# Optimization experiments

Hardware: AMD Instinct MI355X
Metric: run time of the kernel (lower is better)

Reference implementation:

```python
import jax, jax.numpy as jnp
import numpy as np

N, B, T, D = 4, 4, 512, 512
H, DK, DV = 8, 64, 64
LN_EPS = 1e-5


def setup_inputs() -> dict:
    key = jax.random.key(0)
    ks = jax.random.split(key, 5)
    s = 1.0 / np.sqrt(D)
    return {
        "x": jax.random.normal(ks[0], (N, B, T, D), jnp.float32),
        "Wq": jax.random.normal(ks[1], (D, H * DK), jnp.float32) * s,
        "bq": jnp.zeros((H * DK,), jnp.float32),
        "Wk": jax.random.normal(ks[2], (D, H * DK), jnp.float32) * s,
        "bk": jnp.zeros((H * DK,), jnp.float32),
        "Wv": jax.random.normal(ks[3], (D, H * DV), jnp.float32) * s,
        "bv": jnp.zeros((H * DV,), jnp.float32),
        "Wo": jax.random.normal(ks[4], (H * DV, D), jnp.float32) * (1.0 / np.sqrt(H * DV)),
        "bo": jnp.zeros((D,), jnp.float32),
        "gamma": jnp.ones((D,), jnp.float32),
        "beta": jnp.zeros((D,), jnp.float32),
    }


def reference(x, Wq, bq, Wk, bk, Wv, bv, Wo, bo, gamma, beta):
    # x: [N, B, T, D] -- N variables, each [B, T, D]
    n = x.shape[0]
    # Project once per variable (the torch code redundantly recomputes K/V per query var).
    q = (x @ Wq + bq).reshape(n, B, T, H, DK).transpose(0, 1, 3, 2, 4)  # [N,B,H,T,DK]
    k = (x @ Wk + bk).reshape(n, B, T, H, DK).transpose(0, 1, 3, 2, 4)  # [N,B,H,T,DK]
    v = (x @ Wv + bv).reshape(n, B, T, H, DV).transpose(0, 1, 3, 2, 4)  # [N,B,H,T,DV]
    # All-pairs attention: softmax over keys of EACH key-variable separately.
    scores = jnp.einsum('qbhtk,cbhsk->qcbhts', q, k) / np.sqrt(DK)  # [Nq,Nc,B,H,T,T]
    attn = jax.nn.softmax(scores, axis=-1)
    ctx = jnp.einsum('qcbhts,cbhsv->qcbhtv', attn, v)  # [Nq,Nc,B,H,T,DV]
    ctx = ctx.transpose(0, 1, 2, 4, 3, 5).reshape(n, n, B, T, H * DV)
    out = ctx @ Wo + bo                     # per-pair output projection
    out = out.sum(axis=1) / n               # average over key variables -> [N,B,T,D]
    res = x + out
    mu = res.mean(axis=-1, keepdims=True)
    var = res.var(axis=-1, keepdims=True)
    y = (res - mu) / jnp.sqrt(var + LN_EPS) * gamma + beta
    return y
```

## Files before the change

### kernel.cpp

```cpp
#include <hip/hip_runtime.h>


typedef __bf16 bf16x8 __attribute__((ext_vector_type(8)));
typedef __bf16 bf16x4 __attribute__((ext_vector_type(4)));
typedef short shortx4 __attribute__((ext_vector_type(4)));
typedef float floatx2 __attribute__((ext_vector_type(2)));
typedef float floatx4 __attribute__((ext_vector_type(4)));
typedef float floatx16 __attribute__((ext_vector_type(16)));
typedef unsigned short ushortx8 __attribute__((ext_vector_type(8)));
typedef unsigned int uintx4 __attribute__((ext_vector_type(4)));

static __device__ __forceinline__ unsigned short f2bf(float f) {
  union { __bf16 h; unsigned short u; } c; c.h = (__bf16)f; return c.u;
}
static __device__ __forceinline__ float bf2f(unsigned short u) {
  union { unsigned u32; float f; } c; c.u32 = ((unsigned)u) << 16; return c.f;
}
static __device__ __forceinline__ unsigned cvtpk(float a, float b) {
  unsigned r;
  asm("v_cvt_pk_bf16_f32 %0, %1, %2" : "=v"(r) : "v"(a), "v"(b));
  return r;
}
static __device__ __forceinline__ void barrier_lgkm() {
  asm volatile("s_waitcnt lgkmcnt(0)\n\ts_barrier" ::: "memory");
}

#define QSCALE 0.18033688011112042f
#define SHIFT2 (-17.312340489609306f)

__global__ __launch_bounds__(256) void prep(
    const float* __restrict__ Wq, const float* __restrict__ Wk,
    const float* __restrict__ Wv, const float* __restrict__ Wo,
    const float* __restrict__ x,
    unsigned short* __restrict__ wqkvT, unsigned short* __restrict__ woT,
    unsigned short* __restrict__ x_bf)
{
  const int bid = blockIdx.x;
  const int tid = threadIdx.x;
  if (bid < 256) {
    __shared__ unsigned short lds[64][65];
    const int z = bid >> 6, rest = bid & 63;
    const int k0 = (rest >> 3) * 64, n0 = (rest & 7) * 64;
    const float* W; unsigned short* T;
    if (z == 0)      { W = Wq; T = wqkvT; }
    else if (z == 1) { W = Wk; T = wqkvT + 262144; }
    else if (z == 2) { W = Wv; T = wqkvT + 524288; }
    else             { W = Wo; T = woT; }
    const int xx = tid & 63, yy = tid >> 6;
#pragma unroll
    for (int i = 0; i < 16; ++i) {
      const int row = yy * 16 + i;
      lds[row][xx] = f2bf(W[(size_t)(k0 + row) * 512 + n0 + xx]);
    }
    __syncthreads();
#pragma unroll
    for (int i = 0; i < 16; ++i) {
      const int nr = yy * 16 + i;
      T[(size_t)(n0 + nr) * 512 + k0 + xx] = lds[xx][nr];
    }
  } else {
    const int i = (bid - 256) * 256 + tid;
    const float4 a = ((const float4*)x)[i * 2];
    const float4 b = ((const float4*)x)[i * 2 + 1];
    ushortx8 o;
    o[0] = f2bf(a.x); o[1] = f2bf(a.y); o[2] = f2bf(a.z); o[3] = f2bf(a.w);
    o[4] = f2bf(b.x); o[5] = f2bf(b.y); o[6] = f2bf(b.z); o[7] = f2bf(b.w);
    *(ushortx8*)(x_bf + (size_t)i * 8) = o;
  }
}

__global__ __launch_bounds__(256) void gemm_qkv(
    const unsigned short* __restrict__ Xb,
    const unsigned short* __restrict__ BT,
    const float* __restrict__ bq, const float* __restrict__ bk,
    const float* __restrict__ bv,
    unsigned short* __restrict__ Qo, unsigned short* __restrict__ Ko,
    unsigned short* __restrict__ Vo)
{
  __shared__ __align__(16) unsigned short sbuf[18432];
  auto lA = (unsigned short (*)[72])sbuf;
  auto lB = (unsigned short (*)[72])(sbuf + 9216);
  const int tid  = threadIdx.x;
  const int wv   = tid >> 6, lane = tid & 63;
  const int quad = lane >> 4, l16 = lane & 15;
  const int wm = wv >> 1, wn = wv & 1;
  const int m0  = blockIdx.x * 128;
  const int n0g = blockIdx.y * 128;
  const int sel = n0g >> 9;
  const float* bias = (sel == 0) ? bq : (sel == 1) ? bk : bv;
  const float scale = (sel == 0) ? QSCALE : 1.0f;
  unsigned short* outp = (sel == 0) ? Qo : (sel == 1) ? Ko : Vo;

  floatx4 acc[4][4] = {};
  const int srow = tid >> 1, sc0 = (tid & 1) * 32;

  for (int kc = 0; kc < 512; kc += 64) {
    __syncthreads();
    const unsigned short* as = Xb + (size_t)(m0 + srow) * 512 + kc + sc0;
    const unsigned short* bs = BT + (size_t)(n0g + srow) * 512 + kc + sc0;
#pragma unroll
    for (int j = 0; j < 4; ++j) {
      *(bf16x8*)&lA[srow][sc0 + j * 8] = *(const bf16x8*)(as + j * 8);
      *(bf16x8*)&lB[srow][sc0 + j * 8] = *(const bf16x8*)(bs + j * 8);
    }
    __syncthreads();
    bf16x8 af[4][2];
#pragma unroll
    for (int ti = 0; ti < 4; ++ti) {
      af[ti][0] = *(const bf16x8*)&lA[wm * 64 + ti * 16 + l16][quad * 8];
      af[ti][1] = *(const bf16x8*)&lA[wm * 64 + ti * 16 + l16][32 + quad * 8];
    }
#pragma unroll
    for (int ni = 0; ni < 4; ++ni) {
      bf16x8 b0 = *(const bf16x8*)&lB[wn * 64 + ni * 16 + l16][quad * 8];
      bf16x8 b1 = *(const bf16x8*)&lB[wn * 64 + ni * 16 + l16][32 + quad * 8];
#pragma unroll
      for (int ti = 0; ti < 4; ++ti) {
        acc[ti][ni] = __builtin_amdgcn_mfma_f32_16x16x32_bf16(af[ti][0], b0, acc[ti][ni], 0, 0, 0);
        acc[ti][ni] = __builtin_amdgcn_mfma_f32_16x16x32_bf16(af[ti][1], b1, acc[ti][ni], 0, 0, 0);
      }
    }
  }

  if (sel != 2) {
#pragma unroll
    for (int ni = 0; ni < 4; ++ni) {
      const int n = (n0g & 511) + wn * 64 + ni * 16 + l16;
      const float bvv = bias[n];
      const int hh = n >> 6, dk = n & 63;
#pragma unroll
      for (int ti = 0; ti < 4; ++ti) {
        const int mb = m0 + wm * 64 + ti * 16 + quad * 4;
#pragma unroll
        for (int r = 0; r < 4; ++r) {
          const int m = mb + r;
          const int nb = m >> 9, t = m & 511;
          outp[((size_t)(nb * 8 + hh) * 512 + t) * 64 + dk] =
              f2bf((acc[ti][ni][r] + bvv) * scale);
        }
      }
    }
  } else {
    __syncthreads();
    auto tb = (unsigned short (*)[136])sbuf;
#pragma unroll
    for (int ni = 0; ni < 4; ++ni) {
      const int n = (n0g & 511) + wn * 64 + ni * 16 + l16;
      const float bvv = bias[n];
      const int drow = wn * 64 + ni * 16 + l16;
#pragma unroll
      for (int ti = 0; ti < 4; ++ti) {
        const int tcol = wm * 64 + ti * 16 + quad * 4;
        shortx4 pk;
        pk[0] = (short)f2bf(acc[ti][ni][0] + bvv);
        pk[1] = (short)f2bf(acc[ti][ni][1] + bvv);
        pk[2] = (short)f2bf(acc[ti][ni][2] + bvv);
        pk[3] = (short)f2bf(acc[ti][ni][3] + bvv);
        *(shortx4*)&tb[drow][tcol] = pk;
      }
    }
    __syncthreads();
    const int drow = tid >> 1, th = tid & 1;
    const int n = (n0g & 511) + drow;
    const int hh = n >> 6, dk = n & 63;
    const int nb = m0 >> 9, tbase = (m0 & 511) + th * 64;
    unsigned short* gdst = outp + ((size_t)(nb * 8 + hh) * 64 + dk) * 512 + tbase;
#pragma unroll
    for (int j = 0; j < 8; ++j)
      *(ushortx8*)(gdst + j * 8) = *(const ushortx8*)&tb[drow][th * 64 + j * 8];
  }
}

__global__ __launch_bounds__(256) void gemm_out(
    const unsigned short* __restrict__ C0, const unsigned short* __restrict__ C1,
    const unsigned short* __restrict__ BT, unsigned short* __restrict__ Cout)
{
  __shared__ __align__(16) unsigned short lA[128][72];
  __shared__ __align__(16) unsigned short lB[128][72];
  const int tid  = threadIdx.x;
  const int wv   = tid >> 6, lane = tid & 63;
  const int quad = lane >> 4, l16 = lane & 15;
  const int wm = wv >> 1, wn = wv & 1;
  const int m0 = blockIdx.x * 128, n0 = blockIdx.y * 128;

  floatx4 acc[4][4] = {};
  const int srow = tid >> 1, sc0 = (tid & 1) * 32;

  for (int kc = 0; kc < 512; kc += 64) {
    __syncthreads();
    const size_t aoff = (size_t)(m0 + srow) * 512 + kc + sc0;
    const unsigned short* bs = BT + (size_t)(n0 + srow) * 512 + kc + sc0;
#pragma unroll
    for (int j = 0; j < 4; ++j) {
      ushortx8 a0 = *(const ushortx8*)(C0 + aoff + j * 8);
      ushortx8 a1 = *(const ushortx8*)(C1 + aoff + j * 8);
      ushortx8 o;
#pragma unroll
      for (int e = 0; e < 8; ++e) o[e] = f2bf(bf2f(a0[e]) + bf2f(a1[e]));
      *(ushortx8*)&lA[srow][sc0 + j * 8] = o;
      *(bf16x8*)&lB[srow][sc0 + j * 8] = *(const bf16x8*)(bs + j * 8);
    }
    __syncthreads();
    bf16x8 af[4][2];
#pragma unroll
    for (int ti = 0; ti < 4; ++ti) {
      af[ti][0] = *(const bf16x8*)&lA[wm * 64 + ti * 16 + l16][quad * 8];
      af[ti][1] = *(const bf16x8*)&lA[wm * 64 + ti * 16 + l16][32 + quad * 8];
    }
#pragma unroll
    for (int ni = 0; ni < 4; ++ni) {
      bf16x8 b0 = *(const bf16x8*)&lB[wn * 64 + ni * 16 + l16][quad * 8];
      bf16x8 b1 = *(const bf16x8*)&lB[wn * 64 + ni * 16 + l16][32 + quad * 8];
#pragma unroll
      for (int ti = 0; ti < 4; ++ti) {
        acc[ti][ni] = __builtin_amdgcn_mfma_f32_16x16x32_bf16(af[ti][0], b0, acc[ti][ni], 0, 0, 0);
        acc[ti][ni] = __builtin_amdgcn_mfma_f32_16x16x32_bf16(af[ti][1], b1, acc[ti][ni], 0, 0, 0);
      }
    }
  }

#pragma unroll
  for (int ni = 0; ni < 4; ++ni) {
    const int n = n0 + wn * 64 + ni * 16 + l16;
#pragma unroll
    for (int ti = 0; ti < 4; ++ti) {
      const int mb = m0 + wm * 64 + ti * 16 + quad * 4;
#pragma unroll
      for (int r = 0; r < 4; ++r)
        Cout[(size_t)(mb + r) * 512 + n] = f2bf(acc[ti][ni][r]);
    }
  }
}

__global__ __launch_bounds__(256) void flash_kernel(
    const unsigned short* __restrict__ Q,
    const unsigned short* __restrict__ K,
    const unsigned short* __restrict__ VT,
    unsigned short* __restrict__ CTX2)
{
  __shared__ __align__(16) unsigned short lK[2][64][72];
  __shared__ __align__(16) unsigned short lV[2][64][68];
  const int tid  = threadIdx.x;
  const int wv   = tid >> 6, lane = tid & 63;
  const int l32  = lane & 31, u = lane >> 5;

  const int lin  = blockIdx.x;
  const int xcd  = lin & 7, slot = lin >> 3;
  const int tile = slot & 3;
  const int nbh  = xcd * 16 + ((slot >> 2) & 15);
  const int cg   = slot >> 6;
  const int t0   = tile * 128;
  const int h = nbh & 7, nb = nbh >> 3, b = nb & 3;

  const unsigned short* qbase = Q + ((size_t)nbh * 512 + (t0 + wv * 32 + l32)) * 64;
  bf16x8 qf[4];
#pragma unroll
  for (int c16 = 0; c16 < 4; ++c16)
    qf[c16] = *(const bf16x8*)(qbase + c16 * 16 + u * 8);

  const int srow = tid >> 2, sc0 = (tid & 3) * 16;
  const unsigned short *kptr, *vptr;
  auto setptr = [&](int it) {
    const int c = cg * 2 + (it >> 3), s0 = (it & 7) * 64;
    const size_t kvbh = (size_t)((c * 4 + b) * 8 + h);
    kptr = K  + kvbh * (512 * 64) + (size_t)(s0 + srow) * 64 + sc0;
    vptr = VT + kvbh * (64 * 512) + (size_t)srow * 512 + s0 + sc0;
  };
  bf16x8 rk0, rk1, rv0, rv1;
  auto loadregs = [&]() {
    rk0 = *(const bf16x8*)kptr; rk1 = *(const bf16x8*)(kptr + 8);
    rv0 = *(const bf16x8*)vptr; rv1 = *(const bf16x8*)(vptr + 8);
  };
  auto writebuf = [&](int p) {
    *(bf16x8*)&lK[p][srow][sc0]     = rk0;
    *(bf16x8*)&lK[p][srow][sc0 + 8] = rk1;
    union { bf16x8 v8; bf16x4 v4[2]; } c0, c1;
    c0.v8 = rv0; c1.v8 = rv1;
    *(bf16x4*)&lV[p][srow][sc0]      = c0.v4[0];
    *(bf16x4*)&lV[p][srow][sc0 + 4]  = c0.v4[1];
    *(bf16x4*)&lV[p][srow][sc0 + 8]  = c1.v4[0];
    *(bf16x4*)&lV[p][srow][sc0 + 12] = c1.v4[1];
  };

  setptr(0); loadregs();
  writebuf(0);
  setptr(1); loadregs();
  barrier_lgkm();

  floatx16 ofin0 = {}, ofin1 = {};
  floatx16 oc0, oc1;
  floatx2 lac2;

  for (int it = 0; it < 16; ++it) {
    const int cur = it & 1;
    const int st = it & 7;
    if (st == 0) { oc0 = floatx16{}; oc1 = floatx16{}; lac2 = floatx2{}; }

    if (it < 15) writebuf(cur ^ 1);
    if (it < 14) { setptr(it + 2); loadregs(); }

    __builtin_amdgcn_s_setprio(1);
#pragma unroll
    for (int sb = 0; sb < 2; ++sb) {
      floatx16 sacc;
#pragma unroll
      for (int r = 0; r < 16; ++r) sacc[r] = SHIFT2;
#pragma unroll
      for (int c16 = 0; c16 < 4; ++c16) {
        bf16x8 ak = *(const bf16x8*)&lK[cur][sb * 32 + l32][c16 * 16 + u * 8];
        sacc = __builtin_amdgcn_mfma_f32_32x32x16_bf16(ak, qf[c16], sacc, 0, 0, 0);
      }
#pragma unroll
      for (int g = 0; g < 2; ++g) {
        float e[8];
#pragma unroll
        for (int j = 0; j < 8; ++j) e[j] = __builtin_amdgcn_exp2f(sacc[8 * g + j]);
        floatx2 s01 = floatx2{e[0], e[1]} + floatx2{e[2], e[3]};
        floatx2 s23 = floatx2{e[4], e[5]} + floatx2{e[6], e[7]};
        lac2 += s01 + s23;
        union { unsigned u32[4]; bf16x8 b8; } pf;
        pf.u32[0] = cvtpk(e[0], e[1]);
        pf.u32[1] = cvtpk(e[2], e[3]);
        pf.u32[2] = cvtpk(e[4], e[5]);
        pf.u32[3] = cvtpk(e[6], e[7]);
        const int slA = sb * 32 + g * 16 + u * 4;
        union { shortx4 s4[2]; bf16x8 b8; } va, vb;
        va.s4[0] = *(const shortx4*)&lV[cur][l32][slA];
        va.s4[1] = *(const shortx4*)&lV[cur][l32][slA + 8];
        vb.s4[0] = *(const shortx4*)&lV[cur][32 + l32][slA];
        vb.s4[1] = *(const shortx4*)&lV[cur][32 + l32][slA + 8];
        oc0 = __builtin_amdgcn_mfma_f32_32x32x16_bf16(pf.b8, va.b8, oc0, 0, 0, 0);
        oc1 = __builtin_amdgcn_mfma_f32_32x32x16_bf16(pf.b8, vb.b8, oc1, 0, 0, 0);
      }
    }
    __builtin_amdgcn_s_setprio(0);

    if (st == 7) {
      float s = lac2[0] + lac2[1];
      s += __shfl_xor(s, 32);
      const float inv = 1.0f / s;
#pragma unroll
      for (int r = 0; r < 16; ++r) {
        const int trow = (r & 3) + 8 * (r >> 2) + 4 * u;
        const float invr = __shfl(inv, trow);
        ofin0[r] += oc0[r] * invr;
        ofin1[r] += oc1[r] * invr;
      }
    }
    barrier_lgkm();
  }

  unsigned short* outp = CTX2 + (size_t)cg * (8192 * 512);
  const int mbase = nb * 512 + t0 + wv * 32;
#pragma unroll
  for (int r = 0; r < 16; ++r) {
    const int trow = (r & 3) + 8 * (r >> 2) + 4 * u;
    const size_t rowoff = (size_t)(mbase + trow) * 512 + h * 64;
    outp[rowoff + l32]      = f2bf(ofin0[r]);
    outp[rowoff + 32 + l32] = f2bf(ofin1[r]);
  }
}

__global__ __launch_bounds__(256) void ln_kernel(
    const float* __restrict__ x, const unsigned short* __restrict__ tmpb,
    const float* __restrict__ bo, const float* __restrict__ gamma,
    const float* __restrict__ beta, float* __restrict__ out)
{
  const int wv   = threadIdx.x >> 6, lane = threadIdx.x & 63;
  const int row  = blockIdx.x * 4 + wv;
  const int col  = lane * 8;
  const size_t base = (size_t)row * 512 + col;
  const float4 x0 = *(const float4*)(x + base);
  const float4 x1 = *(const float4*)(x + base + 4);
  const ushortx8 t8 = *(const ushortx8*)(tmpb + base);
  const float4 b0 = *(const float4*)(bo + col);
  const float4 b1 = *(const float4*)(bo + col + 4);
  float r[8];
  r[0] = x0.x + 0.25f * bf2f(t8[0]) + b0.x;  r[1] = x0.y + 0.25f * bf2f(t8[1]) + b0.y;
  r[2] = x0.z + 0.25f * bf2f(t8[2]) + b0.z;  r[3] = x0.w + 0.25f * bf2f(t8[3]) + b0.w;
  r[4] = x1.x + 0.25f * bf2f(t8[4]) + b1.x;  r[5] = x1.y + 0.25f * bf2f(t8[5]) + b1.y;
  r[6] = x1.z + 0.25f * bf2f(t8[6]) + b1.z;  r[7] = x1.w + 0.25f * bf2f(t8[7]) + b1.w;
  float s = 0.f, sq = 0.f;
#pragma unroll
  for (int j = 0; j < 8; ++j) { s += r[j]; sq += r[j] * r[j]; }
#pragma unroll
  for (int off = 1; off < 64; off <<= 1) {
    s  += __shfl_xor(s, off);
    sq += __shfl_xor(sq, off);
  }
  const float mu  = s * (1.0f / 512.0f);
  const float var = sq * (1.0f / 512.0f) - mu * mu;
  const float inv = rsqrtf(var + 1e-5f);
  const float4 g0 = *(const float4*)(gamma + col);
  const float4 g1 = *(const float4*)(gamma + col + 4);
  const float4 be0 = *(const float4*)(beta + col);
  const float4 be1 = *(const float4*)(beta + col + 4);
  float4 o0, o1;
  o0.x = (r[0] - mu) * inv * g0.x + be0.x;  o0.y = (r[1] - mu) * inv * g0.y + be0.y;
  o0.z = (r[2] - mu) * inv * g0.z + be0.z;  o0.w = (r[3] - mu) * inv * g0.w + be0.w;
  o1.x = (r[4] - mu) * inv * g1.x + be1.x;  o1.y = (r[5] - mu) * inv * g1.y + be1.y;
  o1.z = (r[6] - mu) * inv * g1.z + be1.z;  o1.w = (r[7] - mu) * inv * g1.w + be1.w;
  *(float4*)(out + base)     = o0;
  *(float4*)(out + base + 4) = o1;
}

extern "C" void kernel_launch(void* const* d_in, const int* in_sizes, int n_in,
                              void* d_out, int out_size, void* d_ws, size_t ws_size,
                              hipStream_t stream) {
  const float* x     = (const float*)d_in[0];
  const float* Wq    = (const float*)d_in[1];
  const float* bq    = (const float*)d_in[2];
  const float* Wk    = (const float*)d_in[3];
  const float* bk    = (const float*)d_in[4];
  const float* Wv    = (const float*)d_in[5];
  const float* bv    = (const float*)d_in[6];
  const float* Wo    = (const float*)d_in[7];
  const float* bo    = (const float*)d_in[8];
  const float* gamma = (const float*)d_in[9];
  const float* beta  = (const float*)d_in[10];
  float* out = (float*)d_out;

  char* w = (char*)d_ws;
  unsigned short* q_bf  = (unsigned short*)(w);
  unsigned short* k_bf  = (unsigned short*)(w + (size_t)8  * 1024 * 1024);
  unsigned short* vt_bf = (unsigned short*)(w + (size_t)16 * 1024 * 1024);
  unsigned short* x_bf  = (unsigned short*)(w + (size_t)24 * 1024 * 1024);
  unsigned short* ctx2  = (unsigned short*)(w + (size_t)24 * 1024 * 1024);
  unsigned short* wqkvT = (unsigned short*)(w + (size_t)40 * 1024 * 1024);
  unsigned short* woT   = wqkvT + 786432;
  unsigned short* tmpb  = (unsigned short*)(w);

  prep<<<2304, 256, 0, stream>>>(Wq, Wk, Wv, Wo, x, wqkvT, woT, x_bf);
  gemm_qkv<<<dim3(64, 12), 256, 0, stream>>>(x_bf, wqkvT, bq, bk, bv,
                                             q_bf, k_bf, vt_bf);
  flash_kernel<<<1024, 256, 0, stream>>>(q_bf, k_bf, vt_bf, ctx2);
  gemm_out<<<dim3(64, 4), 256, 0, stream>>>(ctx2, ctx2 + (size_t)8192 * 512,
                                            woT, tmpb);
  ln_kernel<<<2048, 256, 0, stream>>>(x, tmpb, bo, gamma, beta, out);
}
```

Measured before the change: 189.3 us.

## Split flash attention per key-variable into 2048 blocks with four-way ctx reduction

When the workspace allows, the flash kernel assigns each block one key variable instead of two, doubling the grid to 2048 blocks. Each block writes its own normalized context slice to one of four buffers. The output GEMM then sums the four bf16 context slices while staging the A tile. This gives more parallelism and a shorter serial loop per block, at the cost of a larger intermediate buffer, more global memory traffic, and an extra bf16 rounding before the sum.

```diff
diff --git a/kernel.cpp b/kernel.cpp
--- a/kernel.cpp
+++ b/kernel.cpp
@@ -171,7 +171,72 @@
   }
 }
 
-__global__ __launch_bounds__(256) void gemm_out(
+__global__ __launch_bounds__(256) void gemm_out4(
+    const unsigned short* __restrict__ C0, const unsigned short* __restrict__ C1,
+    const unsigned short* __restrict__ C2, const unsigned short* __restrict__ C3,
+    const unsigned short* __restrict__ BT, unsigned short* __restrict__ Cout)
+{
+  __shared__ __align__(16) unsigned short lA[128][72];
+  __shared__ __align__(16) unsigned short lB[128][72];
+  const int tid  = threadIdx.x;
+  const int wv   = tid >> 6, lane = tid & 63;
+  const int quad = lane >> 4, l16 = lane & 15;
+  const int wm = wv >> 1, wn = wv & 1;
+  const int m0 = blockIdx.x * 128, n0 = blockIdx.y * 128;
+
+  floatx4 acc[4][4] = {};
+  const int srow = tid >> 1, sc0 = (tid & 1) * 32;
+
+  for (int kc = 0; kc < 512; kc += 64) {
+    __syncthreads();
+    const size_t aoff = (size_t)(m0 + srow) * 512 + kc + sc0;
+    const unsigned short* bs = BT + (size_t)(n0 + srow) * 512 + kc + sc0;
+#pragma unroll
+    for (int j = 0; j < 4; ++j) {
+      ushortx8 a0 = *(const ushortx8*)(C0 + aoff + j * 8);
+      ushortx8 a1 = *(const ushortx8*)(C1 + aoff + j * 8);
+      ushortx8 a2 = *(const ushortx8*)(C2 + aoff + j * 8);
+      ushortx8 a3 = *(const ushortx8*)(C3 + aoff + j * 8);
+      ushortx8 o;
+#pragma unroll
+      for (int e = 0; e < 8; ++e)
+        o[e] = f2bf((bf2f(a0[e]) + bf2f(a1[e])) + (bf2f(a2[e]) + bf2f(a3[e])));
+      *(ushortx8*)&lA[srow][sc0 + j * 8] = o;
+      *(bf16x8*)&lB[srow][sc0 + j * 8] = *(const bf16x8*)(bs + j * 8);
+    }
+    __syncthreads();
+    bf16x8 af[4][2];
+#pragma unroll
+    for (int ti = 0; ti < 4; ++ti) {
+      af[ti][0] = *(const bf16x8*)&lA[wm * 64 + ti * 16 + l16][quad * 8];
+      af[ti][1] = *(const bf16x8*)&lA[wm * 64 + ti * 16 + l16][32 + quad * 8];
+    }
+#pragma unroll
+    for (int ni = 0; ni < 4; ++ni) {
+      bf16x8 b0 = *(const bf16x8*)&lB[wn * 64 + ni * 16 + l16][quad * 8];
+      bf16x8 b1 = *(const bf16x8*)&lB[wn * 64 + ni * 16 + l16][32 + quad * 8];
+#pragma unroll
+      for (int ti = 0; ti < 4; ++ti) {
+        acc[ti][ni] = __builtin_amdgcn_mfma_f32_16x16x32_bf16(af[ti][0], b0, acc[ti][ni], 0, 0, 0);
+        acc[ti][ni] = __builtin_amdgcn_mfma_f32_16x16x32_bf16(af[ti][1], b1, acc[ti][ni], 0, 0, 0);
+      }
+    }
+  }
+
+#pragma unroll
+  for (int ni = 0; ni < 4; ++ni) {
+    const int n = n0 + wn * 64 + ni * 16 + l16;
+#pragma unroll
+    for (int ti = 0; ti < 4; ++ti) {
+      const int mb = m0 + wm * 64 + ti * 16 + quad * 4;
+#pragma unroll
+      for (int r = 0; r < 4; ++r)
+        Cout[(size_t)(mb + r) * 512 + n] = f2bf(acc[ti][ni][r]);
+    }
+  }
+}
+
+__global__ __launch_bounds__(256) void gemm_out2(
     const unsigned short* __restrict__ C0, const unsigned short* __restrict__ C1,
     const unsigned short* __restrict__ BT, unsigned short* __restrict__ Cout)
 {
@@ -232,7 +297,128 @@
   }
 }
 
-__global__ __launch_bounds__(256) void flash_kernel(
+__global__ __launch_bounds__(256) void flash_c1(
+    const unsigned short* __restrict__ Q,
+    const unsigned short* __restrict__ K,
+    const unsigned short* __restrict__ VT,
+    unsigned short* __restrict__ CTX4)
+{
+  __shared__ __align__(16) unsigned short lK[2][64][72];
+  __shared__ __align__(16) unsigned short lV[2][64][68];
+  const int tid  = threadIdx.x;
+  const int wv   = tid >> 6, lane = tid & 63;
+  const int l32  = lane & 31, u = lane >> 5;
+
+  const int lin  = blockIdx.x;
+  const int xcd  = lin & 7, slot = lin >> 3;
+  const int tile = slot & 3;
+  const int nbh  = xcd * 16 + ((slot >> 2) & 15);
+  const int c    = slot >> 6;
+  const int t0   = tile * 128;
+  const int h = nbh & 7, nb = nbh >> 3, b = nb & 3;
+
+  const unsigned short* qbase = Q + ((size_t)nbh * 512 + (t0 + wv * 32 + l32)) * 64;
+  bf16x8 qf[4];
+#pragma unroll
+  for (int c16 = 0; c16 < 4; ++c16)
+    qf[c16] = *(const bf16x8*)(qbase + c16 * 16 + u * 8);
+
+  const int srow = tid >> 2, sc0 = (tid & 3) * 16;
+  const size_t kvbh = (size_t)((c * 4 + b) * 8 + h);
+  const unsigned short* kb = K  + kvbh * (512 * 64);
+  const unsigned short* vb = VT + kvbh * (64 * 512);
+  const unsigned short *kptr, *vptr;
+  auto setptr = [&](int it) {
+    const int s0 = it * 64;
+    kptr = kb + (size_t)(s0 + srow) * 64 + sc0;
+    vptr = vb + (size_t)srow * 512 + s0 + sc0;
+  };
+  bf16x8 rk0, rk1, rv0, rv1;
+  auto loadregs = [&]() {
+    rk0 = *(const bf16x8*)kptr; rk1 = *(const bf16x8*)(kptr + 8);
+    rv0 = *(const bf16x8*)vptr; rv1 = *(const bf16x8*)(vptr + 8);
+  };
+  auto writebuf = [&](int p) {
+    *(bf16x8*)&lK[p][srow][sc0]     = rk0;
+    *(bf16x8*)&lK[p][srow][sc0 + 8] = rk1;
+    union { bf16x8 v8; bf16x4 v4[2]; } c0, c1;
+    c0.v8 = rv0; c1.v8 = rv1;
+    *(bf16x4*)&lV[p][srow][sc0]      = c0.v4[0];
+    *(bf16x4*)&lV[p][srow][sc0 + 4]  = c0.v4[1];
+    *(bf16x4*)&lV[p][srow][sc0 + 8]  = c1.v4[0];
+    *(bf16x4*)&lV[p][srow][sc0 + 12] = c1.v4[1];
+  };
+
+  setptr(0); loadregs();
+  writebuf(0);
+  setptr(1); loadregs();
+  barrier_lgkm();
+
+  floatx16 oc0 = {}, oc1 = {};
+  floatx2 lac2 = {};
+
+  for (int it = 0; it < 8; ++it) {
+    const int cur = it & 1;
+
+    if (it < 7) writebuf(cur ^ 1);
+    if (it < 6) { setptr(it + 2); loadregs(); }
+
+    __builtin_amdgcn_s_setprio(1);
+#pragma unroll
+    for (int sb = 0; sb < 2; ++sb) {
+      floatx16 sacc;
+#pragma unroll
+      for (int r = 0; r < 16; ++r) sacc[r] = SHIFT2;
+#pragma unroll
+      for (int c16 = 0; c16 < 4; ++c16) {
+        bf16x8 ak = *(const bf16x8*)&lK[cur][sb * 32 + l32][c16 * 16 + u * 8];
+        sacc = __builtin_amdgcn_mfma_f32_32x32x16_bf16(ak, qf[c16], sacc, 0, 0, 0);
+      }
+#pragma unroll
+      for (int g = 0; g < 2; ++g) {
+        float e[8];
+#pragma unroll
+        for (int j = 0; j < 8; ++j) e[j] = __builtin_amdgcn_exp2f(sacc[8 * g + j]);
+        floatx2 s01 = floatx2{e[0], e[1]} + floatx2{e[2], e[3]};
+        floatx2 s23 = floatx2{e[4], e[5]} + floatx2{e[6], e[7]};
+        lac2 += s01 + s23;
+        union { unsigned u32[4]; bf16x8 b8; } pf;
+        pf.u32[0] = cvtpk(e[0], e[1]);
+        pf.u32[1] = cvtpk(e[2], e[3]);
+        pf.u32[2] = cvtpk(e[4], e[5]);
+        pf.u32[3] = cvtpk(e[6], e[7]);
+        const int slA = sb * 32 + g * 16 + u * 4;
+        union { shortx4 s4[2]; bf16x8 b8; } va, vb2;
+        va.s4[0]  = *(const shortx4*)&lV[cur][l32][slA];
+        va.s4[1]  = *(const shortx4*)&lV[cur][l32][slA + 8];
+        vb2.s4[0] = *(const shortx4*)&lV[cur][32 + l32][slA];
+        vb2.s4[1] = *(const shortx4*)&lV[cur][32 + l32][slA + 8];
+        oc0 = __builtin_amdgcn_mfma_f32_32x32x16_bf16(pf.b8, va.b8,  oc0, 0, 0, 0);
+        oc1 = __builtin_amdgcn_mfma_f32_32x32x16_bf16(pf.b8, vb2.b8, oc1, 0, 0, 0);
+      }
+    }
+    __builtin_amdgcn_s_setprio(0);
+
+    if (it < 7) barrier_lgkm();
+  }
+
+  float s = lac2[0] + lac2[1];
+  s += __shfl_xor(s, 32);
+  const float inv = 1.0f / s;
+
+  unsigned short* outp = CTX4 + (size_t)c * (8192 * 512);
+  const int mbase = nb * 512 + t0 + wv * 32;
+#pragma unroll
+  for (int r = 0; r < 16; ++r) {
+    const int trow = (r & 3) + 8 * (r >> 2) + 4 * u;
+    const float invr = __shfl(inv, trow);
+    const size_t rowoff = (size_t)(mbase + trow) * 512 + h * 64;
+    outp[rowoff + l32]      = f2bf(oc0[r] * invr);
+    outp[rowoff + 32 + l32] = f2bf(oc1[r] * invr);
+  }
+}
+
+__global__ __launch_bounds__(256) void flash_c2(
     const unsigned short* __restrict__ Q,
     const unsigned short* __restrict__ K,
     const unsigned short* __restrict__ VT,
@@ -421,20 +607,42 @@
   float* out = (float*)d_out;
 
   char* w = (char*)d_ws;
-  unsigned short* q_bf  = (unsigned short*)(w);
-  unsigned short* k_bf  = (unsigned short*)(w + (size_t)8  * 1024 * 1024);
-  unsigned short* vt_bf = (unsigned short*)(w + (size_t)16 * 1024 * 1024);
-  unsigned short* x_bf  = (unsigned short*)(w + (size_t)24 * 1024 * 1024);
-  unsigned short* ctx2  = (unsigned short*)(w + (size_t)24 * 1024 * 1024);
-  unsigned short* wqkvT = (unsigned short*)(w + (size_t)40 * 1024 * 1024);
-  unsigned short* woT   = wqkvT + 786432;
-  unsigned short* tmpb  = (unsigned short*)(w);
-
-  prep<<<2304, 256, 0, stream>>>(Wq, Wk, Wv, Wo, x, wqkvT, woT, x_bf);
-  gemm_qkv<<<dim3(64, 12), 256, 0, stream>>>(x_bf, wqkvT, bq, bk, bv,
-                                             q_bf, k_bf, vt_bf);
-  flash_kernel<<<1024, 256, 0, stream>>>(q_bf, k_bf, vt_bf, ctx2);
-  gemm_out<<<dim3(64, 4), 256, 0, stream>>>(ctx2, ctx2 + (size_t)8192 * 512,
-                                            woT, tmpb);
-  ln_kernel<<<2048, 256, 0, stream>>>(x, tmpb, bo, gamma, beta, out);
-}
+  const size_t MB = 1024 * 1024;
+
+  if (ws_size >= 58 * MB) {
+    unsigned short* q_bf  = (unsigned short*)(w);
+    unsigned short* k_bf  = (unsigned short*)(w + 8 * MB);
+    unsigned short* vt_bf = (unsigned short*)(w + 16 * MB);
+    unsigned short* x_bf  = (unsigned short*)(w + 24 * MB);
+    unsigned short* ctx4  = (unsigned short*)(w + 24 * MB);
+    unsigned short* wqkvT = (unsigned short*)(w + 56 * MB);
+    unsigned short* woT   = wqkvT + 786432;
+    unsigned short* tmpb  = (unsigned short*)(w);
+
+    prep<<<2304, 256, 0, stream>>>(Wq, Wk, Wv, Wo, x, wqkvT, woT, x_bf);
+    gemm_qkv<<<dim3(64, 12), 256, 0, stream>>>(x_bf, wqkvT, bq, bk, bv,
+                                               q_bf, k_bf, vt_bf);
+    flash_c1<<<2048, 256, 0, stream>>>(q_bf, k_bf, vt_bf, ctx4);
+    gemm_out4<<<dim3(64, 4), 256, 0, stream>>>(
+        ctx4, ctx4 + (size_t)8192 * 512, ctx4 + (size_t)2 * 8192 * 512,
+        ctx4 + (size_t)3 * 8192 * 512, woT, tmpb);
+    ln_kernel<<<2048, 256, 0, stream>>>(x, tmpb, bo, gamma, beta, out);
+  } else {
+    unsigned short* q_bf  = (unsigned short*)(w);
+    unsigned short* k_bf  = (unsigned short*)(w + 8 * MB);
+    unsigned short* vt_bf = (unsigned short*)(w + 16 * MB);
+    unsigned short* x_bf  = (unsigned short*)(w + 24 * MB);
+    unsigned short* ctx2  = (unsigned short*)(w + 24 * MB);
+    unsigned short* wqkvT = (unsigned short*)(w + 40 * MB);
+    unsigned short* woT   = wqkvT + 786432;
+    unsigned short* tmpb  = (unsigned short*)(w);
+
+    prep<<<2304, 256, 0, stream>>>(Wq, Wk, Wv, Wo, x, wqkvT, woT, x_bf);
+    gemm_qkv<<<dim3(64, 12), 256, 0, stream>>>(x_bf, wqkvT, bq, bk, bv,
+                                               q_bf, k_bf, vt_bf);
+    flash_c2<<<1024, 256, 0, stream>>>(q_bf, k_bf, vt_bf, ctx2);
+    gemm_out2<<<dim3(64, 4), 256, 0, stream>>>(ctx2, ctx2 + (size_t)8192 * 512,
+                                               woT, tmpb);
+    ln_kernel<<<2048, 256, 0, stream>>>(x, tmpb, bo, gamma, beta, out);
+  }
+}
```

New measurement: 206.5 us. 9.1% more time.
